# Optimization experiments

Hardware: AMD Instinct MI355X
Metric: run time of the kernel (lower is better)

Reference implementation:

```python
import jax, jax.numpy as jnp
import numpy as np

N, E, IN_DIM, HID, HEADS, LAYERS, NTYPES, NGRAPH = 50000, 600000, 64, 128, 8, 3, 10, 500
C = HID // HEADS
NEG_SLOPE = 0.2
EPS = 1e-5


def setup_inputs() -> dict:
    key = jax.random.key(0)
    ks = jax.random.split(key, 24)
    inp = {
        "x": jax.random.normal(ks[0], (N, IN_DIM), jnp.float32),
        "edge_index": jax.random.randint(ks[1], (2, E), 0, N),
        "node_types": jax.random.randint(ks[2], (N,), 0, NTYPES),
        "batch": jnp.sort(jax.random.randint(ks[3], (N,), 0, NGRAPH)),
        # node embedding linear
        "emb_W": jax.random.normal(ks[4], (IN_DIM, HID), jnp.float32) / np.sqrt(IN_DIM),
        "emb_b": jnp.zeros((HID,), jnp.float32),
        "ntype_emb": jax.random.normal(ks[5], (NTYPES, HID), jnp.float32) * 0.02,
        # stacked GAT layer params
        "gat_W": jax.random.normal(ks[6], (LAYERS, HID, HID), jnp.float32) / np.sqrt(HID),
        "att_src": jax.random.normal(ks[7], (LAYERS, HEADS, C), jnp.float32) * 0.1,
        "att_dst": jax.random.normal(ks[8], (LAYERS, HEADS, C), jnp.float32) * 0.1,
        "gat_b": jnp.zeros((LAYERS, HID), jnp.float32),
        "ln_g": jnp.ones((LAYERS, HID), jnp.float32),
        "ln_b": jnp.zeros((LAYERS, HID), jnp.float32),
        # global attention MLP
        "ga_W1": jax.random.normal(ks[9], (HID, HID), jnp.float32) / np.sqrt(HID),
        "ga_b1": jnp.zeros((HID,), jnp.float32),
        "ga_W2": jax.random.normal(ks[10], (HID, 1), jnp.float32) / np.sqrt(HID),
        "ga_b2": jnp.zeros((1,), jnp.float32),
        # graph classifier head
        "cls_W1": jax.random.normal(ks[11], (HID, HID), jnp.float32) / np.sqrt(HID),
        "cls_b1": jnp.zeros((HID,), jnp.float32),
        "cls_W2": jax.random.normal(ks[12], (HID, 1), jnp.float32) / np.sqrt(HID),
        "cls_b2": jnp.zeros((1,), jnp.float32),
    }
    return inp


def _layer_norm(h, g, b):
    mu = jnp.mean(h, axis=-1, keepdims=True)
    var = jnp.mean(jnp.square(h - mu), axis=-1, keepdims=True)
    return (h - mu) * jax.lax.rsqrt(var + EPS) * g + b


def _gat_layer(h, src, dst, W, a_src, a_dst, bias):
    # h: [N, HID] -> per-head projection [N, H, C]
    hp = (h @ W).reshape(N, HEADS, C)
    alpha_s = jnp.sum(hp * a_src, axis=-1)  # [N, H]
    alpha_d = jnp.sum(hp * a_dst, axis=-1)  # [N, H]
    e = jax.nn.leaky_relu(alpha_s[src] + alpha_d[dst], NEG_SLOPE)  # [E', H]
    # segment softmax over incoming edges of each destination node
    m = jax.ops.segment_max(e, dst, num_segments=N)
    ex = jnp.exp(e - m[dst])
    s = jax.ops.segment_sum(ex, dst, num_segments=N)
    alpha = ex / s[dst]  # every node has a self-loop, so s > 0
    msg = hp[src] * alpha[:, :, None]  # [E', H, C]
    out = jax.ops.segment_sum(msg, dst, num_segments=N)  # [N, H, C]
    return out.reshape(N, HID) + bias


def reference(x, edge_index, node_types, batch, emb_W, emb_b, ntype_emb,
              gat_W, att_src, att_dst, gat_b, ln_g, ln_b,
              ga_W1, ga_b1, ga_W2, ga_b2, cls_W1, cls_b1, cls_W2, cls_b2):
    # self-loops (PyG GATConv add_self_loops=True)
    loop = jnp.arange(N)
    src = jnp.concatenate([edge_index[0], loop])
    dst = jnp.concatenate([edge_index[1], loop])

    h = x @ emb_W + emb_b
    h = h + ntype_emb[node_types]

    for l in range(LAYERS):
        h_prev = h
        h = _gat_layer(h, src, dst, gat_W[l], att_src[l], att_dst[l], gat_b[l])
        h = _layer_norm(h, ln_g[l], ln_b[l])
        h = jax.nn.relu(h + h_prev)

    # global attention pooling: softmax over all nodes (dim 0, as in source)
    scores = jnp.tanh(h @ ga_W1 + ga_b1) @ ga_W2 + ga_b2  # [N, 1]
    attw = jax.nn.softmax(scores, axis=0)
    h_graph = jnp.sum(h * attw, axis=0)  # [HID]

    # global mean pool per graph
    sums = jax.ops.segment_sum(h, batch, num_segments=NGRAPH)  # [G, HID]
    cnts = jax.ops.segment_sum(jnp.ones((N, 1), h.dtype), batch, num_segments=NGRAPH)
    mean_pool = sums / jnp.maximum(cnts, 1.0)

    hg = h_graph + mean_pool  # broadcast [HID] + [G, HID]

    # graph classifier head (features_batch=None path), squeeze(-1)
    out = jax.nn.relu(hg @ cls_W1 + cls_b1) @ cls_W2 + cls_b2
    return out.squeeze(-1)  # [G]
```

## Files before the change

kernel.cpp:

```cpp
#include <hip/hip_runtime.h>
#include <hip/hip_bf16.h>
#include <math.h>

#define HID 128
#define HEADS 8
#define INDIM 64

typedef _Float16 f16x8 __attribute__((ext_vector_type(8)));
typedef _Float16 f16x4 __attribute__((ext_vector_type(4)));
typedef _Float16 f16x2 __attribute__((ext_vector_type(2)));
typedef float f32x4 __attribute__((ext_vector_type(4)));

__device__ __forceinline__ float fast_tanh(float x) {
    return 1.f - 2.f / (__expf(2.f * x) + 1.f);
}

#if defined(__has_builtin)
#if __has_builtin(__builtin_amdgcn_fdot2)
#define HAVE_FDOT2 1
#endif
#endif

__global__ void prologue_kernel(const int* __restrict__ ei, int* __restrict__ deg,
                                const float* __restrict__ emb_W, const float* __restrict__ gat_W,
                                const float* __restrict__ ga_W1, _Float16* __restrict__ wt_emb,
                                _Float16* __restrict__ wt_gat, _Float16* __restrict__ wt_ga1,
                                const int* __restrict__ batch, int* __restrict__ gstart,
                                float* __restrict__ hgZ,
                                int E, int EE, int N, int G) {
    int i = blockIdx.x * blockDim.x + threadIdx.x;
    if (i < EE) {
        int dst = (i < E) ? ei[E + i] : (i - E);
        atomicAdd(&deg[dst], 1);
    }
    if (i < 8192) {
        int k = i >> 7, n = i & 127;
        wt_emb[n * 64 + k] = (_Float16)emb_W[i];
    } else if (i < 8192 + 49152) {
        int j = i - 8192;
        int l = j >> 14, r = j & 16383;
        int k = r >> 7, n = r & 127;
        wt_gat[l * 16384 + n * 128 + k] = (_Float16)gat_W[j];
    } else if (i < 73728) {
        int j = i - 57344;
        int k = j >> 7, n = j & 127;
        wt_ga1[n * 128 + k] = (_Float16)ga_W1[j];
    } else if (i < 73728 + 129) {
        hgZ[i - 73728] = 0.f;
    }
    if (i >= 100000 && i - 100000 <= G) {
        int g = i - 100000;
        int lo = 0, hi = N;
        while (lo < hi) {
            int mid = (lo + hi) >> 1;
            if (batch[mid] < g) lo = mid + 1; else hi = mid;
        }
        gstart[g] = lo;
    }
}

__global__ __launch_bounds__(256) void mfma_proj_kernel(
    int mode, int K, int N,
    const _Float16* __restrict__ A16, const float* __restrict__ Af32,
    const _Float16* __restrict__ Wt,
    const float* __restrict__ bias, const float* __restrict__ nemb,
    const int* __restrict__ ntypes, _Float16* __restrict__ h16out,
    const float* __restrict__ asrc, const float* __restrict__ adst,
    _Float16* __restrict__ hp_out, float* __restrict__ als, float* __restrict__ ald,
    const float* __restrict__ w2, const float* __restrict__ b2,
    float* __restrict__ escore,
    int PB, int task, const int* __restrict__ ei2,
    const int* __restrict__ degc,
    int* __restrict__ rowptrw, int* __restrict__ woffw, int* __restrict__ esrcw,
    int E2, int EE2)
{
    __shared__ _Float16 w_lds[128 * 136];
    __shared__ _Float16 a_lds[64 * 136];
    int t = threadIdx.x;

    if ((int)blockIdx.x >= PB) {
        if (task == 1) {
            int b = (int)blockIdx.x - PB;
            int i = b * 256 + t;
            int v = (i < N) ? degc[i] : 0;
            int pe = 0;
            for (int j = t; j < (b << 8); j += 256) pe += degc[j];
#pragma unroll
            for (int m = 32; m >= 1; m >>= 1) pe += __shfl_xor(pe, m, 64);
            int* itmp  = (int*)a_lds;
            int* itmp2 = itmp + 256;
            itmp[t] = v;
            if ((t & 63) == 0) itmp2[t >> 6] = pe;
            __syncthreads();
#pragma unroll
            for (int off = 1; off < 256; off <<= 1) {
                int x = (t >= off) ? itmp[t - off] : 0;
                __syncthreads();
                itmp[t] += x;
                __syncthreads();
            }
            pe = itmp2[0] + itmp2[1] + itmp2[2] + itmp2[3];
            int excl = itmp[t] - v + pe;
            if (i < N) { rowptrw[i] = excl; woffw[i] = excl; }
            if (b == 0 && t == 0) rowptrw[N] = EE2;
        } else {
            int sb = (int)blockIdx.x - PB;
            int stride = ((int)gridDim.x - PB) << 8;
            for (int e = sb * 256 + t; e < EE2; e += stride) {
                int src, dst;
                if (e < E2) { src = ei2[e]; dst = ei2[E2 + e]; } else { src = dst = e - E2; }
                int slot = atomicAdd(&woffw[dst], 1);
                esrcw[slot] = src;
            }
        }
        return;
    }

    int KP = K + 8;
    int K8 = K >> 3;

    for (int i = t; i < 128 * K8; i += 256) {
        int row = i / K8, c8 = i - row * K8;
        *(f16x8*)&w_lds[row * KP + 8 * c8] = *(const f16x8*)&Wt[(size_t)row * K + 8 * c8];
    }

    int lane = t & 63, wv = t >> 6;
    int l15 = lane & 15, quad = lane >> 4;

    for (int tile = 0; tile < 2; ++tile) {
        int n0 = blockIdx.x * 128 + tile * 64;
        if (n0 >= N) break;
        __syncthreads();
        if (mode == 0) {
            for (int i = t; i < 64 * K8; i += 256) {
                int row = i / K8, c8 = i - row * K8;
                f16x8 v = {};
                int n = n0 + row;
                if (n < N) {
                    const float4* p = (const float4*)&Af32[(size_t)n * K + 8 * c8];
                    float4 a = p[0], b = p[1];
                    v[0] = (_Float16)a.x; v[1] = (_Float16)a.y;
                    v[2] = (_Float16)a.z; v[3] = (_Float16)a.w;
                    v[4] = (_Float16)b.x; v[5] = (_Float16)b.y;
                    v[6] = (_Float16)b.z; v[7] = (_Float16)b.w;
                }
                *(f16x8*)&a_lds[row * KP + 8 * c8] = v;
            }
        } else {
            for (int i = t; i < 64 * K8; i += 256) {
                int row = i / K8, c8 = i - row * K8;
                f16x8 v = {};
                if (n0 + row < N) v = *(const f16x8*)&A16[(size_t)(n0 + row) * K + 8 * c8];
                *(f16x8*)&a_lds[row * KP + 8 * c8] = v;
            }
        }
        __syncthreads();

        f32x4 acc[8];
#pragma unroll
        for (int c = 0; c < 8; ++c) acc[c] = (f32x4){0.f, 0.f, 0.f, 0.f};

        int ksteps = K >> 5;
        for (int kk = 0; kk < ksteps; ++kk) {
            f16x8 af = *(const f16x8*)&a_lds[(wv * 16 + l15) * KP + kk * 32 + quad * 8];
#pragma unroll
            for (int c = 0; c < 8; ++c) {
                f16x8 bf = *(const f16x8*)&w_lds[(c * 16 + l15) * KP + kk * 32 + quad * 8];
                acc[c] = __builtin_amdgcn_mfma_f32_16x16x32_f16(af, bf, acc[c], 0, 0, 0);
            }
        }

        if (mode == 0) {
            float bv[8];
#pragma unroll
            for (int c = 0; c < 8; ++c) bv[c] = bias[c * 16 + l15];
            __syncthreads();
#pragma unroll
            for (int r = 0; r < 4; ++r) {
                int n = n0 + wv * 16 + quad * 4 + r;
                int nt = (n < N) ? ntypes[n] : 0;
#pragma unroll
                for (int c = 0; c < 8; ++c)
                    a_lds[(wv * 16 + quad * 4 + r) * 136 + c * 16 + l15] =
                        (_Float16)(acc[c][r] + bv[c] + nemb[nt * HID + c * 16 + l15]);
            }
            __syncthreads();
            for (int i = t; i < 64 * 16; i += 256) {
                int row = i >> 4, c8 = i & 15;
                int n = n0 + row;
                if (n < N) *(f16x8*)&h16out[(size_t)n * HID + 8 * c8] = *(const f16x8*)&a_lds[row * 136 + 8 * c8];
            }
        } else if (mode == 1) {
            __syncthreads();
#pragma unroll
            for (int c = 0; c < 8; ++c)
#pragma unroll
                for (int r = 0; r < 4; ++r)
                    a_lds[(wv * 16 + quad * 4 + r) * 136 + c * 16 + l15] = (_Float16)acc[c][r];
            __syncthreads();
            for (int i = t; i < 64 * 16; i += 256) {
                int row = i >> 4, c8 = i & 15;
                int n = n0 + row;
                if (n < N) *(f16x8*)&hp_out[(size_t)n * HID + 8 * c8] = *(const f16x8*)&a_lds[row * 136 + 8 * c8];
            }
            for (int task2 = t; task2 < 512; task2 += 256) {
                int row = task2 >> 3, hd = task2 & 7;
                int n = n0 + row;
                if (n >= N) continue;
                f16x8 v0 = *(const f16x8*)&a_lds[row * 136 + hd * 16];
                f16x8 v1 = *(const f16x8*)&a_lds[row * 136 + hd * 16 + 8];
                float va = 0.f, vd = 0.f;
#pragma unroll
                for (int j = 0; j < 8; ++j) {
                    va += (float)v0[j] * asrc[hd * 16 + j] + (float)v1[j] * asrc[hd * 16 + 8 + j];
                    vd += (float)v0[j] * adst[hd * 16 + j] + (float)v1[j] * adst[hd * 16 + 8 + j];
                }
                als[n * HEADS + hd] = va;
                ald[n * HEADS + hd] = vd;
            }
        } else {
            float b2v = b2[0];
            float treg[4] = {0.f, 0.f, 0.f, 0.f};
#pragma unroll
            for (int c = 0; c < 8; ++c) {
                float b1v = bias[c * 16 + l15];
                float w2v = w2[c * 16 + l15];
#pragma unroll
                for (int r = 0; r < 4; ++r)
                    treg[r] += fast_tanh(acc[c][r] + b1v) * w2v;
            }
#pragma unroll
            for (int r = 0; r < 4; ++r) {
                float v = treg[r];
#pragma unroll
                for (int m = 8; m >= 1; m >>= 1) v += __shfl_xor(v, m, 64);
                if (l15 == 0) {
                    int n = n0 + wv * 16 + quad * 4 + r;
                    if (n < N) escore[n] = __expf(v + b2v);
                }
            }
        }
    }
}

__global__ void gat_aggregate_kernel(const int* __restrict__ rowptr, const int* __restrict__ esrc,
                                     const float* __restrict__ als, const float* __restrict__ ald,
                                     const _Float16* __restrict__ hp16, const float* __restrict__ gb,
                                     const float* __restrict__ lg, const float* __restrict__ lb,
                                     _Float16* __restrict__ h16, int N) {
    int wave = threadIdx.x >> 6;
    int lane = threadIdx.x & 63;
    int n = blockIdx.x * 4 + wave;
    if (n >= N) return;
    int esub = lane >> 4;
    int cg = lane & 15;
    int hd = cg >> 1;
    float adv = ald[n * HEADS + hd];
    int row = rowptr[n], end = rowptr[n + 1];
    int last = end - 1;
    float acc[8] = {0.f, 0.f, 0.f, 0.f, 0.f, 0.f, 0.f, 0.f};
    float sw = 0.f;
    for (int base = row; base < end; base += 16) {
        int iA = base + esub;
        int iB = iA + 4, iC = iA + 8, iD = iA + 12;
        int cA = iA <= last ? iA : last;
        int cB = iB <= last ? iB : last;
        int cC = iC <= last ? iC : last;
        int cD = iD <= last ? iD : last;
        int sA = esrc[cA], sB = esrc[cB], sC = esrc[cC], sD = esrc[cD];
        f16x8 pA = *(const f16x8*)&hp16[(size_t)sA * HID + cg * 8];
        f16x8 pB = *(const f16x8*)&hp16[(size_t)sB * HID + cg * 8];
        f16x8 pC = *(const f16x8*)&hp16[(size_t)sC * HID + cg * 8];
        f16x8 pD = *(const f16x8*)&hp16[(size_t)sD * HID + cg * 8];
        float aA = als[sA * HEADS + hd];
        float aB = als[sB * HEADS + hd];
        float aC = als[sC * HEADS + hd];
        float aD = als[sD * HEADS + hd];
        float lA = aA + adv; lA = lA > 0.f ? lA : 0.2f * lA;
        float lB = aB + adv; lB = lB > 0.f ? lB : 0.2f * lB;
        float lC = aC + adv; lC = lC > 0.f ? lC : 0.2f * lC;
        float lD = aD + adv; lD = lD > 0.f ? lD : 0.2f * lD;
        float wA = __expf(lA) * ((iA < end) ? 1.f : 0.f);
        float wB = __expf(lB) * ((iB < end) ? 1.f : 0.f);
        float wC = __expf(lC) * ((iC < end) ? 1.f : 0.f);
        float wD = __expf(lD) * ((iD < end) ? 1.f : 0.f);
        sw += (wA + wB) + (wC + wD);
#ifdef HAVE_FDOT2
        f16x2 wAB; wAB[0] = (_Float16)wA; wAB[1] = (_Float16)wB;
        f16x2 wCD; wCD[0] = (_Float16)wC; wCD[1] = (_Float16)wD;
#pragma unroll
        for (int j = 0; j < 8; ++j) {
            f16x2 prAB; prAB[0] = pA[j]; prAB[1] = pB[j];
            f16x2 prCD; prCD[0] = pC[j]; prCD[1] = pD[j];
            acc[j] = __builtin_amdgcn_fdot2(prAB, wAB, acc[j], false);
            acc[j] = __builtin_amdgcn_fdot2(prCD, wCD, acc[j], false);
        }
#else
#pragma unroll
        for (int j = 0; j < 8; ++j)
            acc[j] += wA * (float)pA[j] + wB * (float)pB[j]
                    + wC * (float)pC[j] + wD * (float)pD[j];
#endif
    }
#pragma unroll
    for (int m = 16; m <= 32; m <<= 1) {
        sw += __shfl_xor(sw, m, 64);
#pragma unroll
        for (int j = 0; j < 8; ++j) acc[j] += __shfl_xor(acc[j], m, 64);
    }
    float inv_sw = 1.f / sw;
    float4 g0 = ((const float4*)(gb + cg * 8))[0];
    float4 g1 = ((const float4*)(gb + cg * 8))[1];
    float v[8];
    v[0] = acc[0] * inv_sw + g0.x; v[1] = acc[1] * inv_sw + g0.y;
    v[2] = acc[2] * inv_sw + g0.z; v[3] = acc[3] * inv_sw + g0.w;
    v[4] = acc[4] * inv_sw + g1.x; v[5] = acc[5] * inv_sw + g1.y;
    v[6] = acc[6] * inv_sw + g1.z; v[7] = acc[7] * inv_sw + g1.w;
    float s = 0.f;
#pragma unroll
    for (int j = 0; j < 8; ++j) s += v[j];
#pragma unroll
    for (int m = 32; m >= 1; m >>= 1) s += __shfl_xor(s, m, 64);
    float mu = s * (1.f / 512.f);
    float d[8], sq = 0.f;
#pragma unroll
    for (int j = 0; j < 8; ++j) { d[j] = v[j] - mu; sq += d[j] * d[j]; }
#pragma unroll
    for (int m = 32; m >= 1; m >>= 1) sq += __shfl_xor(sq, m, 64);
    float inv = rsqrtf(sq * (1.f / 512.f) + 1e-5f);
    float4 lg0 = ((const float4*)(lg + cg * 8))[0];
    float4 lg1 = ((const float4*)(lg + cg * 8))[1];
    float4 lb0 = ((const float4*)(lb + cg * 8))[0];
    float4 lb1 = ((const float4*)(lb + cg * 8))[1];
    float lgv[8] = {lg0.x, lg0.y, lg0.z, lg0.w, lg1.x, lg1.y, lg1.z, lg1.w};
    float lbv[8] = {lb0.x, lb0.y, lb0.z, lb0.w, lb1.x, lb1.y, lb1.z, lb1.w};
    f16x8 hold = *(const f16x8*)&h16[(size_t)n * HID + cg * 8];
    f16x8 hnew;
#pragma unroll
    for (int j = 0; j < 8; ++j) {
        float r = d[j] * inv * lgv[j] + lbv[j] + (float)hold[j];
        hnew[j] = (_Float16)(r > 0.f ? r : 0.f);
    }
    if (esub == 0) *(f16x8*)&h16[(size_t)n * HID + cg * 8] = hnew;
}

__global__ void pool_graph_kernel(const _Float16* __restrict__ h16, const float* __restrict__ escore,
                                  const int* __restrict__ gstart, float* __restrict__ sums,
                                  float* __restrict__ cnts, float* __restrict__ hgZ, int G) {
    int g = blockIdx.x;
    int t = threadIdx.x;
    int c = t & 127, grp = t >> 7;
    int s = gstart[g], e = gstart[g + 1];
    float msum = 0.f, asum = 0.f, z = 0.f;
    for (int n = s + grp; n < e; n += 4) {
        float hv = (float)h16[(size_t)n * HID + c];
        float es = escore[n];
        msum += hv;
        asum += es * hv;
        if (c == 0) z += es;
    }
    __shared__ float sm[4][HID];
    __shared__ float sa[4][HID];
    __shared__ float sz[4];
    sm[grp][c] = msum;
    sa[grp][c] = asum;
    if (c == 0) sz[grp] = z;
    __syncthreads();
    if (t < HID) {
        float m = sm[0][t] + sm[1][t] + sm[2][t] + sm[3][t];
        float a = sa[0][t] + sa[1][t] + sa[2][t] + sa[3][t];
        sums[(size_t)g * HID + t] = m;
        atomicAdd(&hgZ[t], a);
    } else if (t == HID) {
        cnts[g] = (float)(e - s);
        atomicAdd(&hgZ[HID], sz[0] + sz[1] + sz[2] + sz[3]);
    }
}

__global__ void head_kernel(const float* __restrict__ hgZ, const float* __restrict__ sums,
                            const float* __restrict__ cnts, const float* __restrict__ W1,
                            const float* __restrict__ b1, const float* __restrict__ W2,
                            const float* __restrict__ b2, float* __restrict__ out, int G) {
    int g = blockIdx.x;
    int t = threadIdx.x;
    __shared__ float hr[HID];
    __shared__ float part[2];
    float Z = hgZ[HID];
    float cnt = cnts[g];
    cnt = cnt > 1.f ? cnt : 1.f;
    hr[t] = hgZ[t] / Z + sums[(size_t)g * HID + t] / cnt;
    __syncthreads();
    float acc = b1[t];
#pragma unroll 8
    for (int k = 0; k < HID; ++k) acc += hr[k] * W1[k * HID + t];
    acc = acc > 0.f ? acc : 0.f;
    float v = acc * W2[t];
#pragma unroll
    for (int m = 32; m >= 1; m >>= 1) v += __shfl_xor(v, m, 64);
    if ((t & 63) == 0) part[t >> 6] = v;
    __syncthreads();
    if (t == 0) out[g] = part[0] + part[1] + b2[0];
}

extern "C" void kernel_launch(void* const* d_in, const int* in_sizes, int n_in,
                              void* d_out, int out_size, void* d_ws, size_t ws_size,
                              hipStream_t stream) {
    const float* x        = (const float*)d_in[0];
    const int*   ei       = (const int*)d_in[1];
    const int*   ntypes   = (const int*)d_in[2];
    const int*   batch    = (const int*)d_in[3];
    const float* emb_W    = (const float*)d_in[4];
    const float* emb_b    = (const float*)d_in[5];
    const float* nemb     = (const float*)d_in[6];
    const float* gat_W    = (const float*)d_in[7];
    const float* att_src  = (const float*)d_in[8];
    const float* att_dst  = (const float*)d_in[9];
    const float* gat_b    = (const float*)d_in[10];
    const float* ln_g     = (const float*)d_in[11];
    const float* ln_b     = (const float*)d_in[12];
    const float* ga_W1    = (const float*)d_in[13];
    const float* ga_b1    = (const float*)d_in[14];
    const float* ga_W2    = (const float*)d_in[15];
    const float* ga_b2    = (const float*)d_in[16];
    const float* cls_W1   = (const float*)d_in[17];
    const float* cls_b1   = (const float*)d_in[18];
    const float* cls_W2   = (const float*)d_in[19];
    const float* cls_b2   = (const float*)d_in[20];
    float* out = (float*)d_out;

    const int N  = in_sizes[2];
    const int E  = in_sizes[1] / 2;
    const int EE = E + N;
    const int G  = out_size;
    const int NB = (N + 255) / 256;

    float* ws      = (float*)d_ws;
    float* als     = ws;
    float* ald     = als + (size_t)N * HEADS;
    float* escore  = ald + (size_t)N * HEADS;
    float* sums    = escore + N;
    float* cnts    = sums + (size_t)G * HID;
    float* hgZ     = cnts + G;
    _Float16* h16  = (_Float16*)(hgZ + HID + 1);
    _Float16* hp16 = h16 + (size_t)N * HID;
    _Float16* wt_emb = hp16 + (size_t)N * HID;
    _Float16* wt_gat = wt_emb + 128 * 64;
    _Float16* wt_ga1 = wt_gat + 3 * 128 * 128;
    int*   rowptr  = (int*)(wt_ga1 + 128 * 128);
    int*   woff    = rowptr + (N + 1);
    int*   deg     = woff + N;
    int*   esrc    = deg + N;
    int*   gstart  = esrc + EE;

    hipMemsetAsync(deg, 0, (size_t)N * sizeof(int), stream);
    int ptot = EE;
    if (ptot < 100000 + G + 1) ptot = 100000 + G + 1;
    prologue_kernel<<<(ptot + 255) / 256, 256, 0, stream>>>(
        ei, deg, emb_W, gat_W, ga_W1, wt_emb, wt_gat, wt_ga1,
        batch, gstart, hgZ, E, EE, N, G);

    const int PB = (N + 127) / 128;
    int SCB = 768 - PB;
    if (SCB < 128) SCB = 128;

    mfma_proj_kernel<<<PB + NB, 256, 0, stream>>>(
        0, INDIM, N, nullptr, x, wt_emb, emb_b, nemb, ntypes, h16,
        nullptr, nullptr, nullptr, nullptr, nullptr, nullptr, nullptr, nullptr,
        PB, 1, nullptr, deg, rowptr, woff, nullptr, E, EE);

    mfma_proj_kernel<<<PB + SCB, 256, 0, stream>>>(
        1, HID, N, h16, nullptr, wt_gat,
        nullptr, nullptr, nullptr, nullptr,
        att_src, att_dst, hp16, als, ald, nullptr, nullptr, nullptr,
        PB, 2, ei, nullptr, nullptr, woff, esrc, E, EE);

    gat_aggregate_kernel<<<(N + 3) / 4, 256, 0, stream>>>(
        rowptr, esrc, als, ald, hp16,
        gat_b, ln_g, ln_b, h16, N);

    for (int l = 1; l < 3; ++l) {
        mfma_proj_kernel<<<PB, 256, 0, stream>>>(
            1, HID, N, h16, nullptr, wt_gat + (size_t)l * HID * HID,
            nullptr, nullptr, nullptr, nullptr,
            att_src + l * HID, att_dst + l * HID,
            hp16, als, ald, nullptr, nullptr, nullptr,
            PB, 0, nullptr, nullptr, nullptr, nullptr, nullptr, 0, 0);
        gat_aggregate_kernel<<<(N + 3) / 4, 256, 0, stream>>>(
            rowptr, esrc, als, ald, hp16,
            gat_b + l * HID, ln_g + l * HID, ln_b + l * HID, h16, N);
    }

    mfma_proj_kernel<<<PB, 256, 0, stream>>>(
        2, HID, N, h16, nullptr, wt_ga1, ga_b1, nullptr, nullptr, nullptr,
        nullptr, nullptr, nullptr, nullptr, nullptr, ga_W2, ga_b2, escore,
        PB, 0, nullptr, nullptr, nullptr, nullptr, nullptr, 0, 0);

    pool_graph_kernel<<<G, 512, 0, stream>>>(h16, escore, gstart, sums, cnts, hgZ, G);
    head_kernel<<<G, 128, 0, stream>>>(hgZ, sums, cnts, cls_W1, cls_b1, cls_W2, cls_b2, out, G);
}
```

Baseline: 403.7 us.

## Fuse next-layer projection and attention scoring into GAT aggregation kernel

The aggregation kernel now computes the following layer's linear projection, attention logits, or the global-attention score directly from the freshly normalized node row. It does this with wave shuffles and fdot2 against the fp16 weight in global memory. The separate MFMA projection launches and the extra read of the node features are removed. Ping-pong buffers for projected features and logits avoid read/write hazards. In exchange, the dense matmul runs as a per-node scalar dot-product loop instead of MFMA tiles.

```diff
diff --git a/kernel.cpp b/kernel.cpp
--- a/kernel.cpp
+++ b/kernel.cpp
@@ -10,6 +10,8 @@
 typedef _Float16 f16x4 __attribute__((ext_vector_type(4)));
 typedef _Float16 f16x2 __attribute__((ext_vector_type(2)));
 typedef float f32x4 __attribute__((ext_vector_type(4)));
+
+union F16x8u { f16x8 v; int4 i; f16x2 p[4]; };
 
 __device__ __forceinline__ float fast_tanh(float x) {
     return 1.f - 2.f / (__expf(2.f * x) + 1.f);
@@ -67,8 +69,6 @@
     const int* __restrict__ ntypes, _Float16* __restrict__ h16out,
     const float* __restrict__ asrc, const float* __restrict__ adst,
     _Float16* __restrict__ hp_out, float* __restrict__ als, float* __restrict__ ald,
-    const float* __restrict__ w2, const float* __restrict__ b2,
-    float* __restrict__ escore,
     int PB, int task, const int* __restrict__ ei2,
     const int* __restrict__ degc,
     int* __restrict__ rowptrw, int* __restrict__ woffw, int* __restrict__ esrcw,
@@ -137,12 +137,12 @@
                 f16x8 v = {};
                 int n = n0 + row;
                 if (n < N) {
-                    const float4* p = (const float4*)&Af32[(size_t)n * K + 8 * c8];
-                    float4 a = p[0], b = p[1];
+                    const float4* ptr = (const float4*)&Af32[(size_t)n * K + 8 * c8];
+                    float4 a = ptr[0], b4 = ptr[1];
                     v[0] = (_Float16)a.x; v[1] = (_Float16)a.y;
                     v[2] = (_Float16)a.z; v[3] = (_Float16)a.w;
-                    v[4] = (_Float16)b.x; v[5] = (_Float16)b.y;
-                    v[6] = (_Float16)b.z; v[7] = (_Float16)b.w;
+                    v[4] = (_Float16)b4.x; v[5] = (_Float16)b4.y;
+                    v[6] = (_Float16)b4.z; v[7] = (_Float16)b4.w;
                 }
                 *(f16x8*)&a_lds[row * KP + 8 * c8] = v;
             }
@@ -190,7 +190,7 @@
                 int n = n0 + row;
                 if (n < N) *(f16x8*)&h16out[(size_t)n * HID + 8 * c8] = *(const f16x8*)&a_lds[row * 136 + 8 * c8];
             }
-        } else if (mode == 1) {
+        } else {
             __syncthreads();
 #pragma unroll
             for (int c = 0; c < 8; ++c)
@@ -218,36 +218,22 @@
                 als[n * HEADS + hd] = va;
                 ald[n * HEADS + hd] = vd;
             }
-        } else {
-            float b2v = b2[0];
-            float treg[4] = {0.f, 0.f, 0.f, 0.f};
-#pragma unroll
-            for (int c = 0; c < 8; ++c) {
-                float b1v = bias[c * 16 + l15];
-                float w2v = w2[c * 16 + l15];
-#pragma unroll
-                for (int r = 0; r < 4; ++r)
-                    treg[r] += fast_tanh(acc[c][r] + b1v) * w2v;
-            }
-#pragma unroll
-            for (int r = 0; r < 4; ++r) {
-                float v = treg[r];
-#pragma unroll
-                for (int m = 8; m >= 1; m >>= 1) v += __shfl_xor(v, m, 64);
-                if (l15 == 0) {
-                    int n = n0 + wv * 16 + quad * 4 + r;
-                    if (n < N) escore[n] = __expf(v + b2v);
-                }
-            }
-        }
-    }
-}
-
-__global__ void gat_aggregate_kernel(const int* __restrict__ rowptr, const int* __restrict__ esrc,
-                                     const float* __restrict__ als, const float* __restrict__ ald,
-                                     const _Float16* __restrict__ hp16, const float* __restrict__ gb,
-                                     const float* __restrict__ lg, const float* __restrict__ lb,
-                                     _Float16* __restrict__ h16, int N) {
+        }
+    }
+}
+
+__global__ void agg_proj_kernel(
+    const int* __restrict__ rowptr, const int* __restrict__ esrc,
+    const float* __restrict__ als_in, const float* __restrict__ ald_in,
+    const _Float16* __restrict__ hp_in,
+    const float* __restrict__ gb, const float* __restrict__ lg, const float* __restrict__ lb,
+    _Float16* __restrict__ h16,
+    int mode, const _Float16* __restrict__ Wt,
+    const float* __restrict__ asrc, const float* __restrict__ adst,
+    _Float16* __restrict__ hp_out, float* __restrict__ als_out, float* __restrict__ ald_out,
+    const float* __restrict__ b1, const float* __restrict__ w2f, const float* __restrict__ b2,
+    float* __restrict__ escore, int N)
+{
     int wave = threadIdx.x >> 6;
     int lane = threadIdx.x & 63;
     int n = blockIdx.x * 4 + wave;
@@ -255,7 +241,7 @@
     int esub = lane >> 4;
     int cg = lane & 15;
     int hd = cg >> 1;
-    float adv = ald[n * HEADS + hd];
+    float adv = ald_in[n * HEADS + hd];
     int row = rowptr[n], end = rowptr[n + 1];
     int last = end - 1;
     float acc[8] = {0.f, 0.f, 0.f, 0.f, 0.f, 0.f, 0.f, 0.f};
@@ -268,14 +254,14 @@
         int cC = iC <= last ? iC : last;
         int cD = iD <= last ? iD : last;
         int sA = esrc[cA], sB = esrc[cB], sC = esrc[cC], sD = esrc[cD];
-        f16x8 pA = *(const f16x8*)&hp16[(size_t)sA * HID + cg * 8];
-        f16x8 pB = *(const f16x8*)&hp16[(size_t)sB * HID + cg * 8];
-        f16x8 pC = *(const f16x8*)&hp16[(size_t)sC * HID + cg * 8];
-        f16x8 pD = *(const f16x8*)&hp16[(size_t)sD * HID + cg * 8];
-        float aA = als[sA * HEADS + hd];
-        float aB = als[sB * HEADS + hd];
-        float aC = als[sC * HEADS + hd];
-        float aD = als[sD * HEADS + hd];
+        f16x8 pA = *(const f16x8*)&hp_in[(size_t)sA * HID + cg * 8];
+        f16x8 pB = *(const f16x8*)&hp_in[(size_t)sB * HID + cg * 8];
+        f16x8 pC = *(const f16x8*)&hp_in[(size_t)sC * HID + cg * 8];
+        f16x8 pD = *(const f16x8*)&hp_in[(size_t)sD * HID + cg * 8];
+        float aA = als_in[sA * HEADS + hd];
+        float aB = als_in[sB * HEADS + hd];
+        float aC = als_in[sC * HEADS + hd];
+        float aD = als_in[sD * HEADS + hd];
         float lA = aA + adv; lA = lA > 0.f ? lA : 0.2f * lA;
         float lB = aB + adv; lB = lB > 0.f ? lB : 0.2f * lB;
         float lC = aC + adv; lC = lC > 0.f ? lC : 0.2f * lC;
@@ -334,14 +320,66 @@
     float4 lb1 = ((const float4*)(lb + cg * 8))[1];
     float lgv[8] = {lg0.x, lg0.y, lg0.z, lg0.w, lg1.x, lg1.y, lg1.z, lg1.w};
     float lbv[8] = {lb0.x, lb0.y, lb0.z, lb0.w, lb1.x, lb1.y, lb1.z, lb1.w};
-    f16x8 hold = *(const f16x8*)&h16[(size_t)n * HID + cg * 8];
-    f16x8 hnew;
-#pragma unroll
-    for (int j = 0; j < 8; ++j) {
-        float r = d[j] * inv * lgv[j] + lbv[j] + (float)hold[j];
-        hnew[j] = (_Float16)(r > 0.f ? r : 0.f);
-    }
-    if (esub == 0) *(f16x8*)&h16[(size_t)n * HID + cg * 8] = hnew;
+    F16x8u hu;
+    {
+        f16x8 hold = *(const f16x8*)&h16[(size_t)n * HID + cg * 8];
+#pragma unroll
+        for (int j = 0; j < 8; ++j) {
+            float r = d[j] * inv * lgv[j] + lbv[j] + (float)hold[j];
+            hu.v[j] = (_Float16)(r > 0.f ? r : 0.f);
+        }
+    }
+    if (esub == 0) *(f16x8*)&h16[(size_t)n * HID + cg * 8] = hu.v;
+
+    int c0 = lane << 1;
+    float o0 = 0.f, o1 = 0.f;
+#pragma unroll
+    for (int sc = 0; sc < 16; ++sc) {
+        F16x8u hh;
+        hh.i.x = __shfl(hu.i.x, sc, 64);
+        hh.i.y = __shfl(hu.i.y, sc, 64);
+        hh.i.z = __shfl(hu.i.z, sc, 64);
+        hh.i.w = __shfl(hu.i.w, sc, 64);
+        F16x8u w0u, w1u;
+        w0u.v = *(const f16x8*)&Wt[(size_t)c0 * HID + sc * 8];
+        w1u.v = *(const f16x8*)&Wt[(size_t)(c0 + 1) * HID + sc * 8];
+#ifdef HAVE_FDOT2
+#pragma unroll
+        for (int j = 0; j < 4; ++j) {
+            o0 = __builtin_amdgcn_fdot2(hh.p[j], w0u.p[j], o0, false);
+            o1 = __builtin_amdgcn_fdot2(hh.p[j], w1u.p[j], o1, false);
+        }
+#else
+#pragma unroll
+        for (int j = 0; j < 8; ++j) {
+            o0 += (float)hh.v[j] * (float)w0u.v[j];
+            o1 += (float)hh.v[j] * (float)w1u.v[j];
+        }
+#endif
+    }
+
+    if (mode == 1) {
+        _Float16 h0 = (_Float16)o0, h1 = (_Float16)o1;
+        f16x2 hp2; hp2[0] = h0; hp2[1] = h1;
+        *(f16x2*)&hp_out[(size_t)n * HID + c0] = hp2;
+        float pa = (float)h0 * asrc[c0] + (float)h1 * asrc[c0 + 1];
+        float pd = (float)h0 * adst[c0] + (float)h1 * adst[c0 + 1];
+#pragma unroll
+        for (int m = 1; m <= 4; m <<= 1) {
+            pa += __shfl_xor(pa, m, 64);
+            pd += __shfl_xor(pd, m, 64);
+        }
+        if ((lane & 7) == 0) {
+            als_out[n * HEADS + (lane >> 3)] = pa;
+            ald_out[n * HEADS + (lane >> 3)] = pd;
+        }
+    } else {
+        float sc0 = fast_tanh(o0 + b1[c0]) * w2f[c0]
+                  + fast_tanh(o1 + b1[c0 + 1]) * w2f[c0 + 1];
+#pragma unroll
+        for (int m = 32; m >= 1; m >>= 1) sc0 += __shfl_xor(sc0, m, 64);
+        if (lane == 0) escore[n] = __expf(sc0 + b2[0]);
+    }
 }
 
 __global__ void pool_graph_kernel(const _Float16* __restrict__ h16, const float* __restrict__ escore,
@@ -435,15 +473,18 @@
     const int NB = (N + 255) / 256;
 
     float* ws      = (float*)d_ws;
-    float* als     = ws;
-    float* ald     = als + (size_t)N * HEADS;
-    float* escore  = ald + (size_t)N * HEADS;
+    float* als_a   = ws;
+    float* ald_a   = als_a + (size_t)N * HEADS;
+    float* als_b   = ald_a + (size_t)N * HEADS;
+    float* ald_b   = als_b + (size_t)N * HEADS;
+    float* escore  = ald_b + (size_t)N * HEADS;
     float* sums    = escore + N;
     float* cnts    = sums + (size_t)G * HID;
     float* hgZ     = cnts + G;
-    _Float16* h16  = (_Float16*)(hgZ + HID + 1);
-    _Float16* hp16 = h16 + (size_t)N * HID;
-    _Float16* wt_emb = hp16 + (size_t)N * HID;
+    _Float16* h16  = (_Float16*)(hgZ + 136);
+    _Float16* hp_a = h16 + (size_t)N * HID;
+    _Float16* hp_b = hp_a + (size_t)N * HID;
+    _Float16* wt_emb = hp_b + (size_t)N * HID;
     _Float16* wt_gat = wt_emb + 128 * 64;
     _Float16* wt_ga1 = wt_gat + 3 * 128 * 128;
     int*   rowptr  = (int*)(wt_ga1 + 128 * 128);
@@ -452,10 +493,11 @@
     int*   esrc    = deg + N;
     int*   gstart  = esrc + EE;
 
+    int P1TOT = EE;
+    if (P1TOT < 100000 + G + 1) P1TOT = 100000 + G + 1;
+
     hipMemsetAsync(deg, 0, (size_t)N * sizeof(int), stream);
-    int ptot = EE;
-    if (ptot < 100000 + G + 1) ptot = 100000 + G + 1;
-    prologue_kernel<<<(ptot + 255) / 256, 256, 0, stream>>>(
+    prologue_kernel<<<(P1TOT + 255) / 256, 256, 0, stream>>>(
         ei, deg, emb_W, gat_W, ga_W1, wt_emb, wt_gat, wt_ga1,
         batch, gstart, hgZ, E, EE, N, G);
 
@@ -465,35 +507,35 @@
 
     mfma_proj_kernel<<<PB + NB, 256, 0, stream>>>(
         0, INDIM, N, nullptr, x, wt_emb, emb_b, nemb, ntypes, h16,
-        nullptr, nullptr, nullptr, nullptr, nullptr, nullptr, nullptr, nullptr,
+        nullptr, nullptr, nullptr, nullptr, nullptr,
         PB, 1, nullptr, deg, rowptr, woff, nullptr, E, EE);
 
     mfma_proj_kernel<<<PB + SCB, 256, 0, stream>>>(
         1, HID, N, h16, nullptr, wt_gat,
         nullptr, nullptr, nullptr, nullptr,
-        att_src, att_dst, hp16, als, ald, nullptr, nullptr, nullptr,
+        att_src, att_dst, hp_a, als_a, ald_a,
         PB, 2, ei, nullptr, nullptr, woff, esrc, E, EE);
 
-    gat_aggregate_kernel<<<(N + 3) / 4, 256, 0, stream>>>(
-        rowptr, esrc, als, ald, hp16,
-        gat_b, ln_g, ln_b, h16, N);
-
-    for (int l = 1; l < 3; ++l) {
-        mfma_proj_kernel<<<PB, 256, 0, stream>>>(
-            1, HID, N, h16, nullptr, wt_gat + (size_t)l * HID * HID,
-            nullptr, nullptr, nullptr, nullptr,
-            att_src + l * HID, att_dst + l * HID,
-            hp16, als, ald, nullptr, nullptr, nullptr,
-            PB, 0, nullptr, nullptr, nullptr, nullptr, nullptr, 0, 0);
-        gat_aggregate_kernel<<<(N + 3) / 4, 256, 0, stream>>>(
-            rowptr, esrc, als, ald, hp16,
-            gat_b + l * HID, ln_g + l * HID, ln_b + l * HID, h16, N);
-    }
-
-    mfma_proj_kernel<<<PB, 256, 0, stream>>>(
-        2, HID, N, h16, nullptr, wt_ga1, ga_b1, nullptr, nullptr, nullptr,
-        nullptr, nullptr, nullptr, nullptr, nullptr, ga_W2, ga_b2, escore,
-        PB, 0, nullptr, nullptr, nullptr, nullptr, nullptr, 0, 0);
+    agg_proj_kernel<<<(N + 3) / 4, 256, 0, stream>>>(
+        rowptr, esrc, als_a, ald_a, hp_a,
+        gat_b, ln_g, ln_b, h16,
+        1, wt_gat + 16384, att_src + HID, att_dst + HID,
+        hp_b, als_b, ald_b,
+        nullptr, nullptr, nullptr, nullptr, N);
+
+    agg_proj_kernel<<<(N + 3) / 4, 256, 0, stream>>>(
+        rowptr, esrc, als_b, ald_b, hp_b,
+        gat_b + HID, ln_g + HID, ln_b + HID, h16,
+        1, wt_gat + 32768, att_src + 2 * HID, att_dst + 2 * HID,
+        hp_a, als_a, ald_a,
+        nullptr, nullptr, nullptr, nullptr, N);
+
+    agg_proj_kernel<<<(N + 3) / 4, 256, 0, stream>>>(
+        rowptr, esrc, als_a, ald_a, hp_a,
+        gat_b + 2 * HID, ln_g + 2 * HID, ln_b + 2 * HID, h16,
+        2, wt_ga1, nullptr, nullptr,
+        nullptr, nullptr, nullptr,
+        ga_b1, ga_W2, ga_b2, escore, N);
 
     pool_graph_kernel<<<G, 512, 0, stream>>>(h16, escore, gstart, sums, cnts, hgZ, G);
     head_kernel<<<G, 128, 0, stream>>>(hgZ, sums, cnts, cls_W1, cls_b1, cls_W2, cls_b2, out, G);
```

New measurement: 915.5 us. 127% more time.
